# Optimization experiments

Hardware: AMD Instinct MI355X
Metric: run time of the kernel (lower is better)

Reference implementation:

```python
import jax, jax.numpy as jnp
import numpy as np

NUM_HEADS = 16
HEAD_DIM = 64  # hidden_size 1024 / 16 heads


def setup_inputs() -> dict:
    key = jax.random.key(0)
    ks = jax.random.split(key, 7)
    B, S, D = 32, 577, 1024
    s = 0.02
    return {
        "hidden_states": jax.random.normal(ks[0], (B, S, D), dtype=jnp.float32),
        "Wq": jax.random.normal(ks[1], (D, D), dtype=jnp.float32) * s,
        "bq": jax.random.normal(ks[2], (D,), dtype=jnp.float32) * s,
        "Wk": jax.random.normal(ks[3], (D, D), dtype=jnp.float32) * s,
        "bk": jax.random.normal(ks[4], (D,), dtype=jnp.float32) * s,
        "Wv": jax.random.normal(ks[5], (D, D), dtype=jnp.float32) * s,
        "bv": jax.random.normal(ks[6], (D,), dtype=jnp.float32) * s,
    }


def _split_heads(x):
    # [B, S, D] -> [B, H, S, d]
    B, S, D = x.shape
    return x.reshape(B, S, NUM_HEADS, HEAD_DIM).transpose(0, 2, 1, 3)


def reference(hidden_states, Wq, bq, Wk, bk, Wv, bv):
    # torch Linear: y = x @ W^T + b
    q = _split_heads(hidden_states @ Wq.T + bq)  # [B,H,S,d]
    k = _split_heads(hidden_states @ Wk.T + bk)
    v = _split_heads(hidden_states @ Wv.T + bv)

    scale = 1.0 / np.sqrt(HEAD_DIM).astype(np.float32)
    scores = jnp.einsum("bhqd,bhkd->bhqk", q, k) * scale  # [B,H,S,S]
    probs = jax.nn.softmax(scores, axis=-1)
    ctx = jnp.einsum("bhqk,bhkd->bhqd", probs, v)  # [B,H,S,d]
    B, H, S, d = ctx.shape
    ctx = ctx.transpose(0, 2, 1, 3).reshape(B, S, H * d)  # [B,S,D]
    return ctx
```

## Files before the change

kernel.cpp:

```cpp
#include <hip/hip_runtime.h>
#include <stdint.h>

#define NB 32
#define SEQ 577
#define SPAD 640
#define NH 16
#define HD 64
#define DM 1024
#define MTOT (NB * SEQ)

typedef __bf16 bf16x8 __attribute__((ext_vector_type(8)));
typedef float f32x4 __attribute__((ext_vector_type(4)));
typedef unsigned short u16x8 __attribute__((ext_vector_type(8)));
typedef unsigned short u16x4 __attribute__((ext_vector_type(4)));

__device__ __forceinline__ unsigned short f2bf(float f) {
  unsigned int u = __builtin_bit_cast(unsigned int, f);
  return (unsigned short)((u + 0x7FFFu + ((u >> 16) & 1u)) >> 16);
}

__device__ __forceinline__ f32x4 mfma16(bf16x8 a, bf16x8 b, f32x4 c) {
  return __builtin_amdgcn_mfma_f32_16x16x32_bf16(a, b, c, 0, 0, 0);
}

__device__ __forceinline__ void gload16(const unsigned short* g, unsigned short* l) {
  __builtin_amdgcn_global_load_lds(
      (const __attribute__((address_space(1))) unsigned int*)g,
      (__attribute__((address_space(3))) unsigned int*)l, 16, 0, 0);
}

#if __has_builtin(__builtin_amdgcn_exp2f)
#define EXP2(x) __builtin_amdgcn_exp2f(x)
#else
#define EXP2(x) exp2f(x)
#endif

__global__ void cvt_kernel(const float* __restrict__ x,
                           const float* __restrict__ wq,
                           const float* __restrict__ wk,
                           const float* __restrict__ wv,
                           unsigned short* __restrict__ xb,
                           unsigned short* __restrict__ wb) {
  const long long NX = (long long)MTOT * DM;
  long long i = ((long long)blockIdx.x * blockDim.x + threadIdx.x) * 4;
  const float* src;
  unsigned short* dst;
  if (i < NX) {
    src = x + i;
    dst = xb + i;
  } else {
    long long j = i - NX;
    int wsel = (int)(j >> 20);
    long long off = j & 0xFFFFF;
    src = (wsel == 0 ? wq : wsel == 1 ? wk : wv) + off;
    dst = wb + j;
  }
  f32x4 v = *(const f32x4*)src;
  u16x4 o;
  o.x = f2bf(v.x); o.y = f2bf(v.y); o.z = f2bf(v.z); o.w = f2bf(v.w);
  *(u16x4*)dst = o;
}

__global__ __launch_bounds__(256, 2) void qk_gemm(
    const unsigned short* __restrict__ xb, const unsigned short* __restrict__ wb,
    const float* __restrict__ bq, const float* __restrict__ bk,
    unsigned short* __restrict__ qo, unsigned short* __restrict__ ko) {
  const int id = blockIdx.x;
  const int xcd = id & 7;
  const int slot = id >> 3;
  const int m_tile = slot >> 1;
  const int nz = xcd * 2 + (slot & 1);
  const int z = nz >> 3;
  const int n0 = (nz & 7) * 128;
  const int m0 = m_tile * 128;

  __shared__ __align__(16) unsigned short As[128 * 32];
  __shared__ __align__(16) unsigned short Bs[128 * 32];
  const int t = threadIdx.x;
  const unsigned short* W = wb + (size_t)z * (DM * DM);
  const float* bias = (z == 0 ? bq : bk);
  unsigned short* outp = (z == 0 ? qo : ko);

  const int lane = t & 63;
  const int g = lane >> 4, c = lane & 15;
  const int w = t >> 6;
  const int wm = w & 1, wn = w >> 1;

  const int srow = t >> 2;
  const int scol = (t & 3) * 8;
  int ar0 = m0 + srow;      if (ar0 > MTOT - 1) ar0 = MTOT - 1;
  int ar1 = m0 + 64 + srow; if (ar1 > MTOT - 1) ar1 = MTOT - 1;
  const unsigned short* gA0 = xb + (size_t)ar0 * DM + scol;
  const unsigned short* gA1 = xb + (size_t)ar1 * DM + scol;
  const unsigned short* gB0 = W + (size_t)(n0 + srow) * DM + scol;
  const unsigned short* gB1 = W + (size_t)(n0 + 64 + srow) * DM + scol;
  unsigned short* lA0 = As + t * 8;
  unsigned short* lA1 = As + 2048 + t * 8;
  unsigned short* lB0 = Bs + t * 8;
  unsigned short* lB1 = Bs + 2048 + t * 8;

  f32x4 acc[4][4];
#pragma unroll
  for (int mi = 0; mi < 4; mi++)
#pragma unroll
    for (int ni = 0; ni < 4; ni++) acc[mi][ni] = (f32x4)0.0f;

  for (int k0 = 0; k0 < DM; k0 += 32) {
    __syncthreads();
    gload16(gA0 + k0, lA0);
    gload16(gA1 + k0, lA1);
    gload16(gB0 + k0, lB0);
    gload16(gB1 + k0, lB1);
    __syncthreads();
    bf16x8 af[4], bfr[4];
#pragma unroll
    for (int mi = 0; mi < 4; mi++)
      af[mi] = __builtin_bit_cast(
          bf16x8, *(const u16x8*)(As + (wm * 64 + mi * 16 + c) * 32 + g * 8));
#pragma unroll
    for (int ni = 0; ni < 4; ni++)
      bfr[ni] = __builtin_bit_cast(
          bf16x8, *(const u16x8*)(Bs + (wn * 64 + ni * 16 + c) * 32 + g * 8));
#pragma unroll
    for (int mi = 0; mi < 4; mi++)
#pragma unroll
      for (int ni = 0; ni < 4; ni++)
        acc[mi][ni] = mfma16(af[mi], bfr[ni], acc[mi][ni]);
  }

  float bias4[4];
#pragma unroll
  for (int ni = 0; ni < 4; ni++) bias4[ni] = bias[n0 + wn * 64 + ni * 16 + c];

#pragma unroll
  for (int mi = 0; mi < 4; mi++) {
    int mb = m0 + wm * 64 + mi * 16 + g * 4;
#pragma unroll
    for (int r = 0; r < 4; r++) {
      int m = mb + r;
      if (m >= MTOT) continue;
      int bi = m / SEQ;
      int s = m - bi * SEQ;
#pragma unroll
      for (int ni = 0; ni < 4; ni++) {
        int n = n0 + wn * 64 + ni * 16 + c;
        int hh = n >> 6, dd = n & 63;
        outp[(((size_t)bi * NH + hh) * SPAD + s) * HD + dd] =
            f2bf(acc[mi][ni][r] + bias4[ni]);
      }
    }
  }
}

__global__ __launch_bounds__(256, 2) void vt_gemm(
    const unsigned short* __restrict__ xb, const unsigned short* __restrict__ wb,
    const float* __restrict__ bv, unsigned short* __restrict__ vo) {
  const int id = blockIdx.x;
  const int xcd = id & 7;
  const int m_tile = id >> 3;
  const int n0 = xcd * 128;
  const int m0 = m_tile * 128;

  __shared__ __align__(16) unsigned short As[128 * 32];
  __shared__ __align__(16) unsigned short Bs[128 * 32];
  const int t = threadIdx.x;
  const unsigned short* W = wb + (size_t)2 * (DM * DM);

  const int lane = t & 63;
  const int g = lane >> 4, c = lane & 15;
  const int w = t >> 6;
  const int wm = w & 1, wn = w >> 1;

  const int srow = t >> 2;
  const int scol = (t & 3) * 8;
  int ar0 = m0 + srow;      if (ar0 > MTOT - 1) ar0 = MTOT - 1;
  int ar1 = m0 + 64 + srow; if (ar1 > MTOT - 1) ar1 = MTOT - 1;
  const unsigned short* gA0 = xb + (size_t)ar0 * DM + scol;
  const unsigned short* gA1 = xb + (size_t)ar1 * DM + scol;
  const unsigned short* gB0 = W + (size_t)(n0 + srow) * DM + scol;
  const unsigned short* gB1 = W + (size_t)(n0 + 64 + srow) * DM + scol;
  unsigned short* lA0 = As + t * 8;
  unsigned short* lA1 = As + 2048 + t * 8;
  unsigned short* lB0 = Bs + t * 8;
  unsigned short* lB1 = Bs + 2048 + t * 8;

  f32x4 acc[4][4];
#pragma unroll
  for (int mi = 0; mi < 4; mi++)
#pragma unroll
    for (int ni = 0; ni < 4; ni++) acc[mi][ni] = (f32x4)0.0f;

  for (int k0 = 0; k0 < DM; k0 += 32) {
    __syncthreads();
    gload16(gA0 + k0, lA0);
    gload16(gA1 + k0, lA1);
    gload16(gB0 + k0, lB0);
    gload16(gB1 + k0, lB1);
    __syncthreads();
    bf16x8 af[4], bfr[4];
#pragma unroll
    for (int mi = 0; mi < 4; mi++)
      af[mi] = __builtin_bit_cast(
          bf16x8, *(const u16x8*)(As + (wm * 64 + mi * 16 + c) * 32 + g * 8));
#pragma unroll
    for (int ni = 0; ni < 4; ni++)
      bfr[ni] = __builtin_bit_cast(
          bf16x8, *(const u16x8*)(Bs + (wn * 64 + ni * 16 + c) * 32 + g * 8));
#pragma unroll
    for (int mi = 0; mi < 4; mi++)
#pragma unroll
      for (int ni = 0; ni < 4; ni++)
        acc[mi][ni] = mfma16(bfr[ni], af[mi], acc[mi][ni]);
  }

#pragma unroll
  for (int ni = 0; ni < 4; ni++) {
#pragma unroll
    for (int r = 0; r < 4; r++) {
      int n = n0 + wn * 64 + ni * 16 + g * 4 + r;
      int hh = n >> 6, dd = n & 63;
      float bn = bv[n];
#pragma unroll
      for (int mi = 0; mi < 4; mi++) {
        int m = m0 + wm * 64 + mi * 16 + c;
        if (m >= MTOT) continue;
        int bi = m / SEQ;
        int s = m - bi * SEQ;
        vo[(((size_t)bi * NH + hh) * HD + dd) * SPAD + s] =
            f2bf(acc[mi][ni][r] + bn);
      }
    }
  }
}

__global__ __launch_bounds__(256, 4) void attn_kernel(
    const unsigned short* __restrict__ Qb, const unsigned short* __restrict__ Kb,
    const unsigned short* __restrict__ Vt, float* __restrict__ out) {
  __shared__ __align__(16) unsigned short Ks[64 * 64];
  __shared__ __align__(16) unsigned short Vs[80 * 64];
  __shared__ __align__(16) unsigned short Pl[4][16 * 72];
  const int t = threadIdx.x, lane = t & 63, w = t >> 6;
  const int g = lane >> 4, c = lane & 15;

  const int id = blockIdx.x;
  const int xcd = id & 7;
  const int slot = id >> 3;
  const int qt = slot % 10;
  const int pairIdx = slot / 10;
  const int pair = xcd * 64 + pairIdx;
  const int b = pair >> 4;
  const int h = pair & 15;

  const int q0 = qt * 64 + w * 16;
  const size_t bh = (size_t)b * NH + h;
  const unsigned short* Qp = Qb + bh * SPAD * HD;
  const unsigned short* Kp = Kb + bh * SPAD * HD;
  const unsigned short* Vp = Vt + bh * HD * SPAD;

  {
    int rr = t >> 4, col = (t & 15) * 4;
    unsigned short val = (rr == 0) ? (unsigned short)0x3F80 : (unsigned short)0;
    u16x4 v4 = {val, val, val, val};
    *(u16x4*)(Vs + (64 + rr) * 64 + col) = v4;
  }

  bf16x8 qf0 = __builtin_bit_cast(
      bf16x8, *(const u16x8*)(Qp + (size_t)(q0 + c) * HD + g * 8));
  bf16x8 qf1 = __builtin_bit_cast(
      bf16x8, *(const u16x8*)(Qp + (size_t)(q0 + c) * HD + 32 + g * 8));

  const int C0 = t, C1 = t + 256;
  const int r0 = C0 >> 3, cg0 = (C0 & 7) ^ (r0 & 7);
  const int r1 = C1 >> 3, cg1 = (C1 & 7) ^ (r1 & 7);
  const unsigned short* gK0 = Kp + (size_t)(r0 * 8 + cg0) * 8;
  const unsigned short* gK1 = Kp + (size_t)(r1 * 8 + cg1) * 8;
  const unsigned short* gV0 = Vp + (size_t)r0 * SPAD + cg0 * 8;
  const unsigned short* gV1 = Vp + (size_t)r1 * SPAD + cg1 * 8;
  unsigned short* lK0 = Ks + C0 * 8;
  unsigned short* lK1 = Ks + C1 * 8;
  unsigned short* lV0 = Vs + C0 * 8;
  unsigned short* lV1 = Vs + C1 * 8;

  f32x4 oacc[5];
#pragma unroll
  for (int nt = 0; nt < 5; nt++) oacc[nt] = (f32x4)0.0f;
  unsigned short* pl = &Pl[w][0];
  const float SC = 0.125f * 1.44269504f;

  for (int kt = 0; kt < 10; kt++) {
    const int kv0 = kt * 64;
    __syncthreads();
    gload16(gK0 + kv0 * 64, lK0);
    gload16(gK1 + kv0 * 64, lK1);
    gload16(gV0 + kv0, lV0);
    gload16(gV1 + kv0, lV1);
    __syncthreads();

    f32x4 sc[4];
#pragma unroll
    for (int nt = 0; nt < 4; nt++) {
      const int row = nt * 16 + c;
      const unsigned short* kb = Ks + row * 64;
      bf16x8 k0 = __builtin_bit_cast(
          bf16x8, *(const u16x8*)(kb + ((g ^ (row & 7)) * 8)));
      bf16x8 k1 = __builtin_bit_cast(
          bf16x8, *(const u16x8*)(kb + (((4 + g) ^ (row & 7)) * 8)));
      sc[nt] = mfma16(qf0, k0, (f32x4)0.0f);
      sc[nt] = mfma16(qf1, k1, sc[nt]);
    }

    if (kt == 9) {
#pragma unroll
      for (int nt = 0; nt < 4; nt++) {
        const bool valid = (kv0 + nt * 16 + c) < SEQ;
#pragma unroll
        for (int r = 0; r < 4; r++)
          sc[nt][r] = valid ? EXP2(sc[nt][r] * SC) : 0.0f;
      }
    } else {
#pragma unroll
      for (int nt = 0; nt < 4; nt++)
#pragma unroll
        for (int r = 0; r < 4; r++) sc[nt][r] = EXP2(sc[nt][r] * SC);
    }

#pragma unroll
    for (int nt = 0; nt < 4; nt++)
#pragma unroll
      for (int r = 0; r < 4; r++)
        pl[(g * 4 + r) * 72 + nt * 16 + c] = f2bf(sc[nt][r]);
    bf16x8 pa0 = __builtin_bit_cast(bf16x8, *(const u16x8*)(pl + c * 72 + g * 8));
    bf16x8 pa1 =
        __builtin_bit_cast(bf16x8, *(const u16x8*)(pl + c * 72 + 32 + g * 8));

#pragma unroll
    for (int nt = 0; nt < 5; nt++) {
      const int row = nt * 16 + c;
      const unsigned short* vb = Vs + row * 64;
      bf16x8 v0 = __builtin_bit_cast(
          bf16x8, *(const u16x8*)(vb + ((g ^ (row & 7)) * 8)));
      bf16x8 v1 = __builtin_bit_cast(
          bf16x8, *(const u16x8*)(vb + (((4 + g) ^ (row & 7)) * 8)));
      oacc[nt] = mfma16(pa0, v0, oacc[nt]);
      oacc[nt] = mfma16(pa1, v1, oacc[nt]);
    }
  }

#pragma unroll
  for (int r = 0; r < 4; r++) {
    int s = q0 + g * 4 + r;
    if (s >= SEQ) continue;
    float l = __shfl(oacc[4][r], lane & 48, 64);
    float inv = 1.0f / l;
#pragma unroll
    for (int nt = 0; nt < 4; nt++)
      out[((size_t)b * SEQ + s) * DM + h * HD + nt * 16 + c] =
          oacc[nt][r] * inv;
  }
}

extern "C" void kernel_launch(void* const* d_in, const int* in_sizes, int n_in,
                              void* d_out, int out_size, void* d_ws,
                              size_t ws_size, hipStream_t stream) {
  const float* x = (const float*)d_in[0];
  const float* Wq = (const float*)d_in[1];
  const float* bq = (const float*)d_in[2];
  const float* Wk = (const float*)d_in[3];
  const float* bk = (const float*)d_in[4];
  const float* Wv = (const float*)d_in[5];
  const float* bv = (const float*)d_in[6];
  float* out = (float*)d_out;

  const size_t nXB = (size_t)MTOT * DM;
  const size_t nWB = (size_t)3 * DM * DM;
  const size_t nQK = (size_t)NB * NH * SPAD * HD;
  const size_t needed = (nXB + nWB + 3 * nQK) * 2;
  if (ws_size < needed) return;

  unsigned short* xb = (unsigned short*)d_ws;
  unsigned short* wb = xb + nXB;
  unsigned short* Qb = wb + nWB;
  unsigned short* Kb = Qb + nQK;
  unsigned short* Vt = Kb + nQK;

  cvt_kernel<<<21536, 256, 0, stream>>>(x, Wq, Wk, Wv, xb, wb);
  qk_gemm<<<2320, 256, 0, stream>>>(xb, wb, bq, bk, Qb, Kb);
  vt_gemm<<<1160, 256, 0, stream>>>(xb, wb, bv, Vt);
  attn_kernel<<<5120, 256, 0, stream>>>(Qb, Kb, Vt, out);
}
```

Measured before the change: 408.0 us.

## Rewrite Q/K projection GEMM as 256x256 tile, 8-wave pipelined kernel

```diff
diff --git a/kernel.cpp b/kernel.cpp
--- a/kernel.cpp
+++ b/kernel.cpp
@@ -8,6 +8,7 @@
 #define HD 64
 #define DM 1024
 #define MTOT (NB * SEQ)
+#define KT_N 16
 
 typedef __bf16 bf16x8 __attribute__((ext_vector_type(8)));
 typedef float f32x4 __attribute__((ext_vector_type(4)));
@@ -28,6 +29,8 @@
       (const __attribute__((address_space(1))) unsigned int*)g,
       (__attribute__((address_space(3))) unsigned int*)l, 16, 0, 0);
 }
+
+#define BC8(p) __builtin_bit_cast(bf16x8, *(const u16x8*)(p))
 
 #if __has_builtin(__builtin_amdgcn_exp2f)
 #define EXP2(x) __builtin_amdgcn_exp2f(x)
@@ -61,25 +64,205 @@
   *(u16x4*)dst = o;
 }
 
-__global__ __launch_bounds__(256, 2) void qk_gemm(
+__global__ __launch_bounds__(512, 2) void qk_gemm8(
     const unsigned short* __restrict__ xb, const unsigned short* __restrict__ wb,
     const float* __restrict__ bq, const float* __restrict__ bk,
     unsigned short* __restrict__ qo, unsigned short* __restrict__ ko) {
+  __shared__ __align__(16) unsigned short LDS[65536];
   const int id = blockIdx.x;
   const int xcd = id & 7;
-  const int slot = id >> 3;
-  const int m_tile = slot >> 1;
-  const int nz = xcd * 2 + (slot & 1);
-  const int z = nz >> 3;
-  const int n0 = (nz & 7) * 128;
+  const int idx = id >> 3;
+  const int z = xcd >> 2;
+  const int n0 = (xcd & 3) * 256;
+  const int m0 = idx * 256;
+
+  const int t = threadIdx.x;
+  const int lane = t & 63;
+  const int w = t >> 6;
+  const int g = lane >> 4, c = lane & 15;
+  const int wm = w & 1, wn = w >> 1;
+
+  const unsigned short* W = wb + (size_t)z * (DM * DM);
+  const float* bias = z ? bk : bq;
+  unsigned short* outp = z ? ko : qo;
+
+  const int srow = t >> 3;
+  const int schunk = (t & 7) ^ (srow & 7);
+  const unsigned short* gA[4];
+#pragma unroll
+  for (int q = 0; q < 4; q++) {
+    int rg = m0 + q * 64 + srow;
+    if (rg > MTOT - 1) rg = MTOT - 1;
+    gA[q] = xb + (size_t)rg * DM + schunk * 8;
+  }
+  const unsigned short* gB[4];
+#pragma unroll
+  for (int q = 0; q < 4; q++)
+    gB[q] = W + (size_t)(n0 + q * 64 + srow) * DM + schunk * 8;
+
+  const int cx = c & 7;
+  const int ch0 = (g ^ cx) * 8;
+  const int ch1 = ((4 + g) ^ cx) * 8;
+
+  f32x4 acc[8][4];
+#pragma unroll
+  for (int mi = 0; mi < 8; mi++)
+#pragma unroll
+    for (int ni = 0; ni < 4; ni++) acc[mi][ni] = (f32x4)0.0f;
+
+#pragma unroll
+  for (int q = 0; q < 4; q++) gload16(gA[q], LDS + q * 4096 + t * 8);
+#pragma unroll
+  for (int q = 0; q < 4; q++) gload16(gB[q], LDS + 16384 + q * 4096 + t * 8);
+#pragma unroll
+  for (int q = 0; q < 4; q++) gload16(gA[q] + 64, LDS + 32768 + q * 4096 + t * 8);
+#pragma unroll
+  for (int q = 0; q < 4; q++)
+    gload16(gB[q] + 64, LDS + 32768 + 16384 + q * 4096 + t * 8);
+  asm volatile("s_waitcnt vmcnt(8)" ::: "memory");
+  __builtin_amdgcn_sched_barrier(0);
+  __builtin_amdgcn_s_barrier();
+
+  const int rA0 = wm * 128 + c;
+  const int rB0 = wn * 64 + c;
+
+  for (int kt = 0; kt < KT_N; ++kt) {
+    unsigned short* ab = LDS + (kt & 1) * 32768;
+    unsigned short* bb = ab + 16384;
+    const bool st = (kt + 2) < KT_N;
+    const int ko2 = (kt + 2) * 64;
+    bf16x8 af[4][2], bf0[2][2], bf1[2][2];
+
+#pragma unroll
+    for (int mi = 0; mi < 4; mi++) {
+      const unsigned short* rp = ab + (rA0 + mi * 16) * 64;
+      af[mi][0] = BC8(rp + ch0);
+      af[mi][1] = BC8(rp + ch1);
+    }
+#pragma unroll
+    for (int ni = 0; ni < 2; ni++) {
+      const unsigned short* rp = bb + (rB0 + ni * 16) * 64;
+      bf0[ni][0] = BC8(rp + ch0);
+      bf0[ni][1] = BC8(rp + ch1);
+    }
+    __builtin_amdgcn_s_barrier();
+    asm volatile("s_waitcnt lgkmcnt(0)" ::: "memory");
+    __builtin_amdgcn_sched_barrier(0);
+    __builtin_amdgcn_s_setprio(1);
+#pragma unroll
+    for (int mi = 0; mi < 4; mi++)
+#pragma unroll
+      for (int ni = 0; ni < 2; ni++) {
+        acc[mi][ni] = mfma16(af[mi][0], bf0[ni][0], acc[mi][ni]);
+        acc[mi][ni] = mfma16(af[mi][1], bf0[ni][1], acc[mi][ni]);
+      }
+    __builtin_amdgcn_s_setprio(0);
+    __builtin_amdgcn_s_barrier();
+
+#pragma unroll
+    for (int ni = 0; ni < 2; ni++) {
+      const unsigned short* rp = bb + (rB0 + (2 + ni) * 16) * 64;
+      bf1[ni][0] = BC8(rp + ch0);
+      bf1[ni][1] = BC8(rp + ch1);
+    }
+    if (st) {
+      gload16(gA[0] + ko2, ab + 0 * 4096 + t * 8);
+      gload16(gA[2] + ko2, ab + 2 * 4096 + t * 8);
+    }
+    __builtin_amdgcn_s_barrier();
+    asm volatile("s_waitcnt lgkmcnt(0)" ::: "memory");
+    __builtin_amdgcn_sched_barrier(0);
+    __builtin_amdgcn_s_setprio(1);
+#pragma unroll
+    for (int mi = 0; mi < 4; mi++)
+#pragma unroll
+      for (int ni = 0; ni < 2; ni++) {
+        acc[mi][2 + ni] = mfma16(af[mi][0], bf1[ni][0], acc[mi][2 + ni]);
+        acc[mi][2 + ni] = mfma16(af[mi][1], bf1[ni][1], acc[mi][2 + ni]);
+      }
+    __builtin_amdgcn_s_setprio(0);
+    __builtin_amdgcn_s_barrier();
+
+#pragma unroll
+    for (int mi = 0; mi < 4; mi++) {
+      const unsigned short* rp = ab + (rA0 + 64 + mi * 16) * 64;
+      af[mi][0] = BC8(rp + ch0);
+      af[mi][1] = BC8(rp + ch1);
+    }
+    if (st) {
+#pragma unroll
+      for (int q = 0; q < 4; q++) gload16(gB[q] + ko2, bb + q * 4096 + t * 8);
+    }
+    __builtin_amdgcn_s_barrier();
+    asm volatile("s_waitcnt lgkmcnt(0)" ::: "memory");
+    __builtin_amdgcn_sched_barrier(0);
+    __builtin_amdgcn_s_setprio(1);
+#pragma unroll
+    for (int mi = 0; mi < 4; mi++)
+#pragma unroll
+      for (int ni = 0; ni < 2; ni++) {
+        acc[4 + mi][2 + ni] = mfma16(af[mi][0], bf1[ni][0], acc[4 + mi][2 + ni]);
+        acc[4 + mi][2 + ni] = mfma16(af[mi][1], bf1[ni][1], acc[4 + mi][2 + ni]);
+      }
+    __builtin_amdgcn_s_setprio(0);
+    __builtin_amdgcn_s_barrier();
+
+    if (st) {
+      gload16(gA[1] + ko2, ab + 1 * 4096 + t * 8);
+      gload16(gA[3] + ko2, ab + 3 * 4096 + t * 8);
+    }
+    __builtin_amdgcn_s_barrier();
+    __builtin_amdgcn_s_setprio(1);
+#pragma unroll
+    for (int mi = 0; mi < 4; mi++)
+#pragma unroll
+      for (int ni = 0; ni < 2; ni++) {
+        acc[4 + mi][ni] = mfma16(af[mi][0], bf0[ni][0], acc[4 + mi][ni]);
+        acc[4 + mi][ni] = mfma16(af[mi][1], bf0[ni][1], acc[4 + mi][ni]);
+      }
+    __builtin_amdgcn_s_setprio(0);
+    asm volatile("s_waitcnt vmcnt(8)" ::: "memory");
+    __builtin_amdgcn_sched_barrier(0);
+    __builtin_amdgcn_s_barrier();
+  }
+
+  float bias4[4];
+#pragma unroll
+  for (int ni = 0; ni < 4; ni++) bias4[ni] = bias[n0 + wn * 64 + ni * 16 + c];
+
+#pragma unroll
+  for (int mi = 0; mi < 8; mi++) {
+    int mb = m0 + wm * 128 + mi * 16 + g * 4;
+#pragma unroll
+    for (int r = 0; r < 4; r++) {
+      int m = mb + r;
+      if (m >= MTOT) continue;
+      int bi = m / SEQ;
+      int s = m - bi * SEQ;
+#pragma unroll
+      for (int ni = 0; ni < 4; ni++) {
+        int n = n0 + wn * 64 + ni * 16 + c;
+        int hh = n >> 6, dd = n & 63;
+        outp[(((size_t)bi * NH + hh) * SPAD + s) * HD + dd] =
+            f2bf(acc[mi][ni][r] + bias4[ni]);
+      }
+    }
+  }
+}
+
+__global__ __launch_bounds__(256, 2) void vt_gemm(
+    const unsigned short* __restrict__ xb, const unsigned short* __restrict__ wb,
+    const float* __restrict__ bv, unsigned short* __restrict__ vo) {
+  const int id = blockIdx.x;
+  const int xcd = id & 7;
+  const int m_tile = id >> 3;
+  const int n0 = xcd * 128;
   const int m0 = m_tile * 128;
 
   __shared__ __align__(16) unsigned short As[128 * 32];
   __shared__ __align__(16) unsigned short Bs[128 * 32];
   const int t = threadIdx.x;
-  const unsigned short* W = wb + (size_t)z * (DM * DM);
-  const float* bias = (z == 0 ? bq : bk);
-  unsigned short* outp = (z == 0 ? qo : ko);
+  const unsigned short* W = wb + (size_t)2 * (DM * DM);
 
   const int lane = t & 63;
   const int g = lane >> 4, c = lane & 15;
@@ -125,91 +308,6 @@
     for (int mi = 0; mi < 4; mi++)
 #pragma unroll
       for (int ni = 0; ni < 4; ni++)
-        acc[mi][ni] = mfma16(af[mi], bfr[ni], acc[mi][ni]);
-  }
-
-  float bias4[4];
-#pragma unroll
-  for (int ni = 0; ni < 4; ni++) bias4[ni] = bias[n0 + wn * 64 + ni * 16 + c];
-
-#pragma unroll
-  for (int mi = 0; mi < 4; mi++) {
-    int mb = m0 + wm * 64 + mi * 16 + g * 4;
-#pragma unroll
-    for (int r = 0; r < 4; r++) {
-      int m = mb + r;
-      if (m >= MTOT) continue;
-      int bi = m / SEQ;
-      int s = m - bi * SEQ;
-#pragma unroll
-      for (int ni = 0; ni < 4; ni++) {
-        int n = n0 + wn * 64 + ni * 16 + c;
-        int hh = n >> 6, dd = n & 63;
-        outp[(((size_t)bi * NH + hh) * SPAD + s) * HD + dd] =
-            f2bf(acc[mi][ni][r] + bias4[ni]);
-      }
-    }
-  }
-}
-
-__global__ __launch_bounds__(256, 2) void vt_gemm(
-    const unsigned short* __restrict__ xb, const unsigned short* __restrict__ wb,
-    const float* __restrict__ bv, unsigned short* __restrict__ vo) {
-  const int id = blockIdx.x;
-  const int xcd = id & 7;
-  const int m_tile = id >> 3;
-  const int n0 = xcd * 128;
-  const int m0 = m_tile * 128;
-
-  __shared__ __align__(16) unsigned short As[128 * 32];
-  __shared__ __align__(16) unsigned short Bs[128 * 32];
-  const int t = threadIdx.x;
-  const unsigned short* W = wb + (size_t)2 * (DM * DM);
-
-  const int lane = t & 63;
-  const int g = lane >> 4, c = lane & 15;
-  const int w = t >> 6;
-  const int wm = w & 1, wn = w >> 1;
-
-  const int srow = t >> 2;
-  const int scol = (t & 3) * 8;
-  int ar0 = m0 + srow;      if (ar0 > MTOT - 1) ar0 = MTOT - 1;
-  int ar1 = m0 + 64 + srow; if (ar1 > MTOT - 1) ar1 = MTOT - 1;
-  const unsigned short* gA0 = xb + (size_t)ar0 * DM + scol;
-  const unsigned short* gA1 = xb + (size_t)ar1 * DM + scol;
-  const unsigned short* gB0 = W + (size_t)(n0 + srow) * DM + scol;
-  const unsigned short* gB1 = W + (size_t)(n0 + 64 + srow) * DM + scol;
-  unsigned short* lA0 = As + t * 8;
-  unsigned short* lA1 = As + 2048 + t * 8;
-  unsigned short* lB0 = Bs + t * 8;
-  unsigned short* lB1 = Bs + 2048 + t * 8;
-
-  f32x4 acc[4][4];
-#pragma unroll
-  for (int mi = 0; mi < 4; mi++)
-#pragma unroll
-    for (int ni = 0; ni < 4; ni++) acc[mi][ni] = (f32x4)0.0f;
-
-  for (int k0 = 0; k0 < DM; k0 += 32) {
-    __syncthreads();
-    gload16(gA0 + k0, lA0);
-    gload16(gA1 + k0, lA1);
-    gload16(gB0 + k0, lB0);
-    gload16(gB1 + k0, lB1);
-    __syncthreads();
-    bf16x8 af[4], bfr[4];
-#pragma unroll
-    for (int mi = 0; mi < 4; mi++)
-      af[mi] = __builtin_bit_cast(
-          bf16x8, *(const u16x8*)(As + (wm * 64 + mi * 16 + c) * 32 + g * 8));
-#pragma unroll
-    for (int ni = 0; ni < 4; ni++)
-      bfr[ni] = __builtin_bit_cast(
-          bf16x8, *(const u16x8*)(Bs + (wn * 64 + ni * 16 + c) * 32 + g * 8));
-#pragma unroll
-    for (int mi = 0; mi < 4; mi++)
-#pragma unroll
-      for (int ni = 0; ni < 4; ni++)
         acc[mi][ni] = mfma16(bfr[ni], af[mi], acc[mi][ni]);
   }
 
@@ -384,7 +482,7 @@
   unsigned short* Vt = Kb + nQK;
 
   cvt_kernel<<<21536, 256, 0, stream>>>(x, Wq, Wk, Wv, xb, wb);
-  qk_gemm<<<2320, 256, 0, stream>>>(xb, wb, bq, bk, Qb, Kb);
+  qk_gemm8<<<584, 512, 0, stream>>>(xb, wb, bq, bk, Qb, Kb);
   vt_gemm<<<1160, 256, 0, stream>>>(xb, wb, bv, Vt);
   attn_kernel<<<5120, 256, 0, stream>>>(Qb, Kb, Vt, out);
 }
```

Result: no change. 414.7 us (+1.6%).
